# Kernel tuning notes

Hardware: AMD Instinct MI355X
Metric: run time of the kernel (lower is better)

Reference implementation:

```python
import jax, jax.numpy as jnp
import numpy as np

N, E, DIN, DH, DOUT = 50000, 800000, 128, 128, 64


def setup_inputs() -> dict:
    key = jax.random.key(0)
    ks = jax.random.split(key, 10)
    s = 0.05  # keep activations numerically sane
    return {
        "x": jax.random.normal(ks[0], (N, DIN), jnp.float32),
        "edge_index": jax.random.randint(ks[1], (2, E), 0, N, jnp.int64),
        "w_in": jax.random.normal(ks[2], (DIN, DH), jnp.float32) * s,
        "b_in": jnp.zeros((DH,), jnp.float32),
        "w_l0": jax.random.normal(ks[3], (DH, DH), jnp.float32) * s,
        "w_r0": jax.random.normal(ks[4], (DH, DH), jnp.float32) * s,
        "b0": jnp.zeros((DH,), jnp.float32),
        "w_l1": jax.random.normal(ks[5], (DH, DH), jnp.float32) * s,
        "w_r1": jax.random.normal(ks[6], (DH, DH), jnp.float32) * s,
        "b1": jnp.zeros((DH,), jnp.float32),
        "w_l2": jax.random.normal(ks[7], (DH, DOUT), jnp.float32) * s,
        "w_r2": jax.random.normal(ks[8], (DH, DOUT), jnp.float32) * s,
        "b2": jnp.zeros((DOUT,), jnp.float32),
    }


def _sage_conv(x, src, dst, w_l, w_r, b, n_nodes):
    # PyG SAGEConv (mean aggr): out = lin_l(mean_{j in N(i)} x_j) + lin_r(x_i)
    msg = x[src]  # [E, d] gather
    agg = jax.ops.segment_sum(msg, dst, num_segments=n_nodes)
    deg = jax.ops.segment_sum(jnp.ones((src.shape[0],), x.dtype), dst, num_segments=n_nodes)
    agg = agg / jnp.maximum(deg, 1.0)[:, None]  # isolated nodes -> 0
    return agg @ w_l + x @ w_r + b


def reference(x, edge_index, w_in, b_in, w_l0, w_r0, b0, w_l1, w_r1, b1, w_l2, w_r2, b2):
    src, dst = edge_index[0], edge_index[1]
    n = x.shape[0]
    h = x @ w_in + b_in
    inp = h
    h = jax.nn.relu(h)
    # conv 0 (hidden->hidden) + relu + (eval dropout = id) + residual
    h = _sage_conv(h, src, dst, w_l0, w_r0, b0, n)
    h = jax.nn.relu(h) + 0.2 * inp
    # conv 1 (hidden->hidden)
    h = _sage_conv(h, src, dst, w_l1, w_r1, b1, n)
    h = jax.nn.relu(h) + 0.2 * inp
    # conv 2 (hidden->out), no activation/residual
    h = _sage_conv(h, src, dst, w_l2, w_r2, b2, n)
    return jax.nn.log_softmax(h, axis=-1)
```

## Files before the change

kernel.cpp:

```cpp
#include <hip/hip_runtime.h>
#include <stdint.h>

#define NN 50000
#define NE 800000
#define NBIN 196
#define ABLK 196
#define EPB 4082
#define BCAP 6144

typedef __attribute__((ext_vector_type(8))) short short8;
typedef __attribute__((ext_vector_type(4))) float floatx4;

__device__ __forceinline__ uint16_t f2bf(float f){
  union { float f; uint32_t u; } c; c.f = f;
  uint32_t u = c.u + 0x7FFFu + ((c.u >> 16) & 1u);
  return (uint16_t)(u >> 16);
}
__device__ __forceinline__ float bflo(uint32_t v){
  union { uint32_t u; float f; } c; c.u = v << 16; return c.f;
}
__device__ __forceinline__ float bfhi(uint32_t v){
  union { uint32_t u; float f; } c; c.u = v & 0xFFFF0000u; return c.f;
}

#define B_CVT 6250
#define B_HIST ABLK
#define B_PIN 64
#define B_P0  128
#define B_P1  128
#define B_P2  64

__device__ __forceinline__ void pack_one(int idx, const float* __restrict__ wl,
                                         const float* __restrict__ wr,
                                         uint16_t* __restrict__ bp,
                                         int ncolL, int ncolR, int NT){
  int j = idx & 7, lane = (idx >> 3) & 63, rest = idx >> 9;
  int nt = rest % NT, kt = rest / NT;
  int k = kt * 32 + ((lane >> 4) << 3) + j;
  int n = nt * 16 + (lane & 15);
  float v = (n < ncolL) ? wl[k * ncolL + n] : wr[k * ncolR + (n - ncolL)];
  bp[idx] = f2bf(v);
}

__global__ __launch_bounds__(256) void k_prep(const float* __restrict__ x, uint2* __restrict__ xb,
                                              const int* __restrict__ ei, int* __restrict__ histG,
                                              const float* __restrict__ w_in,
                                              const float* __restrict__ w_l0, const float* __restrict__ w_r0,
                                              const float* __restrict__ w_l1, const float* __restrict__ w_r1,
                                              const float* __restrict__ w_l2, const float* __restrict__ w_r2,
                                              uint16_t* __restrict__ bpIn, uint16_t* __restrict__ bp0,
                                              uint16_t* __restrict__ bp1, uint16_t* __restrict__ bp2){
  __shared__ int hsh[NBIN];
  int b = blockIdx.x;
  if (b < B_CVT){
    int i = b * 256 + threadIdx.x;
    if (i < NN * 128 / 4){
      float4 v = ((const float4*)x)[i];
      uint32_t lo = (uint32_t)f2bf(v.x) | ((uint32_t)f2bf(v.y) << 16);
      uint32_t hi = (uint32_t)f2bf(v.z) | ((uint32_t)f2bf(v.w) << 16);
      xb[i] = make_uint2(lo, hi);
    }
    return;
  }
  b -= B_CVT;
  if (b < B_HIST){
    for (int i = threadIdx.x; i < NBIN; i += 256) hsh[i] = 0;
    __syncthreads();
    int base = b * EPB;
    for (int k = threadIdx.x; k < EPB; k += 256){
      int e = base + k;
      if (e < NE) atomicAdd(&hsh[ei[NE + e] >> 8], 1);
    }
    __syncthreads();
    for (int i = threadIdx.x; i < NBIN; i += 256) histG[b * NBIN + i] = hsh[i];
    return;
  }
  b -= B_HIST;
  if (b < B_PIN){ pack_one(b * 256 + threadIdx.x, w_in, w_in, bpIn, 128, 0, 8); return; }
  b -= B_PIN;
  if (b < B_P0){ pack_one(b * 256 + threadIdx.x, w_l0, w_r0, bp0, 128, 128, 16); return; }
  b -= B_P0;
  if (b < B_P1){ pack_one(b * 256 + threadIdx.x, w_l1, w_r1, bp1, 128, 128, 16); return; }
  b -= B_P1;
  pack_one(b * 256 + threadIdx.x, w_l2, w_r2, bp2, 64, 64, 8);
}

__global__ __launch_bounds__(256) void k_scanG(int* __restrict__ histG, int* __restrict__ binStart){
  __shared__ int s[256];
  int t = threadIdx.x;
  int tot = 0;
  if (t < NBIN){
    for (int b = 0; b < ABLK; ++b){
      int v = histG[b * NBIN + t];
      histG[b * NBIN + t] = tot;
      tot += v;
    }
  }
  s[t] = (t < NBIN) ? tot : 0;
  __syncthreads();
  #pragma unroll
  for (int off = 1; off < 256; off <<= 1){
    int u = (t >= off) ? s[t - off] : 0;
    __syncthreads();
    s[t] += u;
    __syncthreads();
  }
  int excl = s[t] - ((t < NBIN) ? tot : 0);
  if (t < NBIN){
    binStart[t] = excl;
    for (int b = 0; b < ABLK; ++b) histG[b * NBIN + t] += excl;
  }
  if (t == 0) binStart[NBIN] = NE;
}

__global__ __launch_bounds__(256) void k_bin(const int* __restrict__ ei, const int* __restrict__ histG,
                                             uint32_t* __restrict__ pairs){
  __shared__ int h[NBIN], loc[NBIN], cur[NBIN], gof[NBIN];
  __shared__ int sc[256];
  __shared__ uint32_t st[EPB];
  int t = threadIdx.x;
  int base = blockIdx.x * EPB;
  for (int i = t; i < NBIN; i += 256) h[i] = 0;
  __syncthreads();
  for (int k = t; k < EPB; k += 256){
    int e = base + k;
    if (e < NE) atomicAdd(&h[ei[NE + e] >> 8], 1);
  }
  __syncthreads();
  int cv = (t < NBIN) ? h[t] : 0;
  sc[t] = cv;
  __syncthreads();
  #pragma unroll
  for (int off = 1; off < 256; off <<= 1){
    int u = (t >= off) ? sc[t - off] : 0;
    __syncthreads();
    sc[t] += u;
    __syncthreads();
  }
  if (t < NBIN){
    int excl = sc[t] - cv;
    loc[t] = excl;
    cur[t] = excl;
    gof[t] = histG[blockIdx.x * NBIN + t];
  }
  __syncthreads();
  for (int k = t; k < EPB; k += 256){
    int e = base + k;
    if (e < NE){
      int d = ei[NE + e];
      int s0 = ei[e];
      int pos = atomicAdd(&cur[d >> 8], 1);
      st[pos] = (uint32_t)s0 | ((uint32_t)d << 16);
    }
  }
  __syncthreads();
  int cnt = min(EPB, NE - base);
  for (int k = t; k < cnt; k += 256){
    uint32_t v = st[k];
    int bin = (int)(v >> 24);
    pairs[gof[bin] + (k - loc[bin])] = v;
  }
}

__global__ __launch_bounds__(256) void k_csr(const uint32_t* __restrict__ pairs, const int* __restrict__ binStart,
                                             int* __restrict__ rowp, uint16_t* __restrict__ colx){
  __shared__ uint32_t pl[BCAP];
  __shared__ uint16_t stg[BCAP];
  __shared__ int h[256], sc[256];
  int i = blockIdx.x, t = threadIdx.x;
  int p0 = binStart[i], p1 = binStart[i + 1];
  int cnt = min(p1 - p0, BCAP);
  for (int k = t; k < cnt; k += 256) pl[k] = pairs[p0 + k];
  h[t] = 0;
  __syncthreads();
  for (int k = t; k < cnt; k += 256) atomicAdd(&h[(pl[k] >> 16) & 255], 1);
  __syncthreads();
  int cv = h[t];
  sc[t] = cv;
  __syncthreads();
  #pragma unroll
  for (int off = 1; off < 256; off <<= 1){
    int u = (t >= off) ? sc[t - off] : 0;
    __syncthreads();
    sc[t] += u;
    __syncthreads();
  }
  int excl = sc[t] - cv;
  int n0 = i << 8;
  int nc = min(256, NN - n0);
  if (t < nc) rowp[n0 + t] = p0 + excl;
  if (i == NBIN - 1 && t == 0) rowp[NN] = NE;
  h[t] = excl;
  __syncthreads();
  for (int k = t; k < cnt; k += 256){
    uint32_t v = pl[k];
    int pos = atomicAdd(&h[(v >> 16) & 255], 1);
    stg[pos] = (uint16_t)(v & 0xFFFFu);
  }
  __syncthreads();
  for (int k = t; k < cnt; k += 256) colx[p0 + k] = stg[k];
}

__global__ __launch_bounds__(256) void k_lin0(const uint16_t* __restrict__ xb,
                                              const uint16_t* __restrict__ BpIn, const float* __restrict__ b_in,
                                              const uint16_t* __restrict__ Bp0, const float* __restrict__ b0,
                                              uint16_t* __restrict__ resb, uint16_t* __restrict__ y0,
                                              uint16_t* __restrict__ z0){
  __shared__ uint16_t ash[16 * 136];
  int lane = threadIdx.x & 63, wave = threadIdx.x >> 6;
  short8 bIn[4][2], bC0[4][4];
  #pragma unroll
  for (int kt = 0; kt < 4; ++kt){
    #pragma unroll
    for (int n = 0; n < 2; ++n)
      bIn[kt][n] = *(const short8*)(BpIn + (size_t)((kt * 8 + wave * 2 + n) * 64 + lane) * 8);
    #pragma unroll
    for (int n = 0; n < 4; ++n)
      bC0[kt][n] = *(const short8*)(Bp0 + (size_t)((kt * 16 + wave * 4 + n) * 64 + lane) * 8);
  }
  int m = lane & 15, quad = lane >> 4;
  int r0 = blockIdx.x * 16;
  const uint16_t* arow = xb + (size_t)(r0 + m) * 128 + quad * 8;
  short8 af[4];
  #pragma unroll
  for (int kt = 0; kt < 4; ++kt) af[kt] = *(const short8*)(arow + kt * 32);
  floatx4 accH[2];
  #pragma unroll
  for (int n = 0; n < 2; ++n) accH[n] = (floatx4){0.f, 0.f, 0.f, 0.f};
  #pragma unroll
  for (int kt = 0; kt < 4; ++kt)
    #pragma unroll
    for (int n = 0; n < 2; ++n)
      accH[n] = __builtin_amdgcn_mfma_f32_16x16x32_bf16(af[kt], bIn[kt][n], accH[n], 0, 0, 0);
  int rbase = r0 + quad * 4;
  #pragma unroll
  for (int n = 0; n < 2; ++n){
    int c = (wave * 2 + n) * 16 + m;
    float bi = b_in[c];
    #pragma unroll
    for (int i = 0; i < 4; ++i){
      float hh = accH[n][i] + bi;
      int row = rbase + i;
      resb[(size_t)row * 128 + c] = f2bf(0.2f * hh);
      ash[(quad * 4 + i) * 136 + c] = f2bf(fmaxf(hh, 0.f));
    }
  }
  __syncthreads();
  short8 af2[4];
  #pragma unroll
  for (int kt = 0; kt < 4; ++kt)
    af2[kt] = *(const short8*)&ash[m * 136 + quad * 8 + kt * 32];
  floatx4 acc[4];
  #pragma unroll
  for (int n = 0; n < 4; ++n) acc[n] = (floatx4){0.f, 0.f, 0.f, 0.f};
  #pragma unroll
  for (int kt = 0; kt < 4; ++kt)
    #pragma unroll
    for (int n = 0; n < 4; ++n)
      acc[n] = __builtin_amdgcn_mfma_f32_16x16x32_bf16(af2[kt], bC0[kt][n], acc[n], 0, 0, 0);
  #pragma unroll
  for (int n = 0; n < 4; ++n){
    int c = (wave * 4 + n) * 16 + m;
    #pragma unroll
    for (int i = 0; i < 4; ++i){
      float v = acc[n][i];
      int row = rbase + i;
      if (c < 128) y0[(size_t)row * 128 + c] = f2bf(v);
      else         z0[(size_t)row * 128 + (c - 128)] = f2bf(v + b0[c - 128]);
    }
  }
}

template<int NTW, int MODE>
__global__ __launch_bounds__(256) void k_gemm(const uint16_t* __restrict__ A, const uint16_t* __restrict__ Bp,
                                              const float* __restrict__ bias,
                                              uint16_t* __restrict__ o0, uint16_t* __restrict__ o1,
                                              float* __restrict__ o2){
  const int NTT = 4 * NTW;
  int lane = threadIdx.x & 63;
  int wave = threadIdx.x >> 6;
  short8 bfrag[4][NTW];
  #pragma unroll
  for (int kt = 0; kt < 4; ++kt)
    #pragma unroll
    for (int n = 0; n < NTW; ++n)
      bfrag[kt][n] = *(const short8*)(Bp + (size_t)((kt * NTT + wave * NTW + n) * 64 + lane) * 8);

  int m = lane & 15, quad = lane >> 4;
  const int nrt = NN / 16;
  for (int rt = blockIdx.x; rt < nrt; rt += gridDim.x){
    int r0 = rt * 16;
    const uint16_t* arow = A + (size_t)(r0 + m) * 128 + quad * 8;
    short8 af[4];
    #pragma unroll
    for (int kt = 0; kt < 4; ++kt) af[kt] = *(const short8*)(arow + kt * 32);
    floatx4 acc[NTW];
    #pragma unroll
    for (int n = 0; n < NTW; ++n) acc[n] = (floatx4){0.f, 0.f, 0.f, 0.f};
    #pragma unroll
    for (int kt = 0; kt < 4; ++kt)
      #pragma unroll
      for (int n = 0; n < NTW; ++n)
        acc[n] = __builtin_amdgcn_mfma_f32_16x16x32_bf16(af[kt], bfrag[kt][n], acc[n], 0, 0, 0);

    int rbase = r0 + quad * 4;
    #pragma unroll
    for (int n = 0; n < NTW; ++n){
      int c = (wave * NTW + n) * 16 + m;
      #pragma unroll
      for (int i = 0; i < 4; ++i){
        float v = acc[n][i];
        int row = rbase + i;
        if (MODE == 1){
          if (c < 128) o0[(size_t)row * 128 + c] = f2bf(v);
          else         o1[(size_t)row * 128 + (c - 128)] = f2bf(v + bias[c - 128]);
        } else {
          if (c < 64) o0[(size_t)row * 64 + c] = f2bf(v);
          else        o2[(size_t)row * 64 + (c - 64)] = v + bias[c - 64];
        }
      }
    }
  }
}

__global__ __launch_bounds__(256) void agg_mid(const uint4* __restrict__ yb, const uint4* __restrict__ zb,
                                               const uint4* __restrict__ resb,
                                               const uint16_t* __restrict__ colx, const int* __restrict__ rowp,
                                               uint4* __restrict__ hb_out){
  int wid = blockIdx.x * 4 + (threadIdx.x >> 6);
  if (wid >= NN) return;
  int lane = threadIdx.x & 63;
  int q = lane >> 4, sub = lane & 15;
  int e0 = rowp[wid], e1 = rowp[wid + 1];
  float a0 = 0.f, a1 = 0.f, a2 = 0.f, a3 = 0.f, a4 = 0.f, a5 = 0.f, a6 = 0.f, a7 = 0.f;
  int e = e0 + q;
  for (; e + 12 < e1; e += 16){
    uint4 v0 = yb[(size_t)colx[e]      * 16 + sub];
    uint4 v1 = yb[(size_t)colx[e + 4]  * 16 + sub];
    uint4 v2 = yb[(size_t)colx[e + 8]  * 16 + sub];
    uint4 v3 = yb[(size_t)colx[e + 12] * 16 + sub];
    a0 += bflo(v0.x) + bflo(v1.x) + bflo(v2.x) + bflo(v3.x);
    a1 += bfhi(v0.x) + bfhi(v1.x) + bfhi(v2.x) + bfhi(v3.x);
    a2 += bflo(v0.y) + bflo(v1.y) + bflo(v2.y) + bflo(v3.y);
    a3 += bfhi(v0.y) + bfhi(v1.y) + bfhi(v2.y) + bfhi(v3.y);
    a4 += bflo(v0.z) + bflo(v1.z) + bflo(v2.z) + bflo(v3.z);
    a5 += bfhi(v0.z) + bfhi(v1.z) + bfhi(v2.z) + bfhi(v3.z);
    a6 += bflo(v0.w) + bflo(v1.w) + bflo(v2.w) + bflo(v3.w);
    a7 += bfhi(v0.w) + bfhi(v1.w) + bfhi(v2.w) + bfhi(v3.w);
  }
  for (; e < e1; e += 4){
    uint4 v = yb[(size_t)colx[e] * 16 + sub];
    a0 += bflo(v.x); a1 += bfhi(v.x); a2 += bflo(v.y); a3 += bfhi(v.y);
    a4 += bflo(v.z); a5 += bfhi(v.z); a6 += bflo(v.w); a7 += bfhi(v.w);
  }
  #pragma unroll
  for (int off = 16; off < 64; off <<= 1){
    a0 += __shfl_xor(a0, off, 64);
    a1 += __shfl_xor(a1, off, 64);
    a2 += __shfl_xor(a2, off, 64);
    a3 += __shfl_xor(a3, off, 64);
    a4 += __shfl_xor(a4, off, 64);
    a5 += __shfl_xor(a5, off, 64);
    a6 += __shfl_xor(a6, off, 64);
    a7 += __shfl_xor(a7, off, 64);
  }
  int deg = e1 - e0;
  float inv = deg > 0 ? 1.f / (float)deg : 0.f;
  if (q == 0){
    uint4 zv = zb[(size_t)wid * 16 + sub];
    uint4 rv = resb[(size_t)wid * 16 + sub];
    float w0 = fmaxf(a0 * inv + bflo(zv.x), 0.f) + bflo(rv.x);
    float w1 = fmaxf(a1 * inv + bfhi(zv.x), 0.f) + bfhi(rv.x);
    float w2 = fmaxf(a2 * inv + bflo(zv.y), 0.f) + bflo(rv.y);
    float w3 = fmaxf(a3 * inv + bfhi(zv.y), 0.f) + bfhi(rv.y);
    float w4 = fmaxf(a4 * inv + bflo(zv.z), 0.f) + bflo(rv.z);
    float w5 = fmaxf(a5 * inv + bfhi(zv.z), 0.f) + bfhi(rv.z);
    float w6 = fmaxf(a6 * inv + bflo(zv.w), 0.f) + bflo(rv.w);
    float w7 = fmaxf(a7 * inv + bfhi(zv.w), 0.f) + bfhi(rv.w);
    uint4 o;
    o.x = (uint32_t)f2bf(w0) | ((uint32_t)f2bf(w1) << 16);
    o.y = (uint32_t)f2bf(w2) | ((uint32_t)f2bf(w3) << 16);
    o.z = (uint32_t)f2bf(w4) | ((uint32_t)f2bf(w5) << 16);
    o.w = (uint32_t)f2bf(w6) | ((uint32_t)f2bf(w7) << 16);
    hb_out[(size_t)wid * 16 + sub] = o;
  }
}

__global__ __launch_bounds__(256) void agg_out(const uint2* __restrict__ yb2, const float* __restrict__ z2,
                                               const uint16_t* __restrict__ colx, const int* __restrict__ rowp,
                                               float* __restrict__ out){
  int wid = blockIdx.x * 4 + (threadIdx.x >> 6);
  if (wid >= NN) return;
  int lane = threadIdx.x & 63;
  int q = lane >> 4, sub = lane & 15;
  int e0 = rowp[wid], e1 = rowp[wid + 1];
  float a0 = 0.f, a1 = 0.f, a2 = 0.f, a3 = 0.f;
  int e = e0 + q;
  for (; e + 12 < e1; e += 16){
    uint2 v0 = yb2[(size_t)colx[e]      * 16 + sub];
    uint2 v1 = yb2[(size_t)colx[e + 4]  * 16 + sub];
    uint2 v2 = yb2[(size_t)colx[e + 8]  * 16 + sub];
    uint2 v3 = yb2[(size_t)colx[e + 12] * 16 + sub];
    a0 += bflo(v0.x) + bflo(v1.x) + bflo(v2.x) + bflo(v3.x);
    a1 += bfhi(v0.x) + bfhi(v1.x) + bfhi(v2.x) + bfhi(v3.x);
    a2 += bflo(v0.y) + bflo(v1.y) + bflo(v2.y) + bflo(v3.y);
    a3 += bfhi(v0.y) + bfhi(v1.y) + bfhi(v2.y) + bfhi(v3.y);
  }
  for (; e < e1; e += 4){
    uint2 v = yb2[(size_t)colx[e] * 16 + sub];
    a0 += bflo(v.x); a1 += bfhi(v.x); a2 += bflo(v.y); a3 += bfhi(v.y);
  }
  #pragma unroll
  for (int off = 16; off < 64; off <<= 1){
    a0 += __shfl_xor(a0, off, 64);
    a1 += __shfl_xor(a1, off, 64);
    a2 += __shfl_xor(a2, off, 64);
    a3 += __shfl_xor(a3, off, 64);
  }
  int deg = e1 - e0;
  float inv = deg > 0 ? 1.f / (float)deg : 0.f;
  float4 zv = ((const float4*)z2)[(size_t)wid * 16 + sub];
  float v0 = a0 * inv + zv.x;
  float v1 = a1 * inv + zv.y;
  float v2 = a2 * inv + zv.z;
  float v3 = a3 * inv + zv.w;
  float mx = fmaxf(fmaxf(v0, v1), fmaxf(v2, v3));
  #pragma unroll
  for (int off = 1; off < 16; off <<= 1) mx = fmaxf(mx, __shfl_xor(mx, off, 64));
  float sm = __expf(v0 - mx) + __expf(v1 - mx) + __expf(v2 - mx) + __expf(v3 - mx);
  #pragma unroll
  for (int off = 1; off < 16; off <<= 1) sm += __shfl_xor(sm, off, 64);
  if (q == 0){
    float ls = __logf(sm);
    float4 o = make_float4((v0 - mx) - ls, (v1 - mx) - ls, (v2 - mx) - ls, (v3 - mx) - ls);
    ((float4*)out)[(size_t)wid * 16 + sub] = o;
  }
}

extern "C" void kernel_launch(void* const* d_in, const int* in_sizes, int n_in,
                              void* d_out, int out_size, void* d_ws, size_t ws_size,
                              hipStream_t stream){
  const float* x    = (const float*)d_in[0];
  const int*   ei   = (const int*)d_in[1];
  const float* w_in = (const float*)d_in[2];
  const float* b_in = (const float*)d_in[3];
  const float* w_l0 = (const float*)d_in[4];
  const float* w_r0 = (const float*)d_in[5];
  const float* b0   = (const float*)d_in[6];
  const float* w_l1 = (const float*)d_in[7];
  const float* w_r1 = (const float*)d_in[8];
  const float* b1   = (const float*)d_in[9];
  const float* w_l2 = (const float*)d_in[10];
  const float* w_r2 = (const float*)d_in[11];
  const float* b2   = (const float*)d_in[12];
  float* out = (float*)d_out;

  char* ws = (char*)d_ws;
  size_t off = 0;
  auto take = [&](size_t bytes) -> char* {
    char* p = ws + off;
    off = (off + bytes + 1023) & ~(size_t)1023;
    return p;
  };
  uint16_t* xb   = (uint16_t*)take((size_t)NN * 128 * 2);
  uint16_t* hb   = (uint16_t*)take((size_t)NN * 128 * 2);
  uint16_t* resb = (uint16_t*)take((size_t)NN * 128 * 2);
  uint16_t* y0   = (uint16_t*)take((size_t)NN * 128 * 2);
  uint16_t* z0   = (uint16_t*)take((size_t)NN * 128 * 2);
  uint32_t* pairs = (uint32_t*)take((size_t)NE * 4);
  uint16_t* colx  = (uint16_t*)take((size_t)NE * 2);
  int* histG    = (int*)take((size_t)NBIN * ABLK * 4);
  int* binStart = (int*)take((size_t)(NBIN + 1) * 4);
  int* rowp     = (int*)take((size_t)(NN + 1) * 4);
  uint16_t* BpIn = (uint16_t*)take(128 * 128 * 2);
  uint16_t* Bp0  = (uint16_t*)take(128 * 256 * 2);
  uint16_t* Bp1  = (uint16_t*)take(128 * 256 * 2);
  uint16_t* Bp2  = (uint16_t*)take(128 * 128 * 2);
  uint16_t* y2 = y0;
  float*    z2 = (float*)z0;
  (void)ws_size; (void)in_sizes; (void)n_in; (void)out_size;

  k_prep<<<B_CVT + B_HIST + B_PIN + B_P0 + B_P1 + B_P2, 256, 0, stream>>>(
      x, (uint2*)xb, ei, histG, w_in, w_l0, w_r0, w_l1, w_r1, w_l2, w_r2, BpIn, Bp0, Bp1, Bp2);

  k_scanG<<<1, 256, 0, stream>>>(histG, binStart);
  k_bin<<<ABLK, 256, 0, stream>>>(ei, histG, pairs);
  k_csr<<<NBIN, 256, 0, stream>>>(pairs, binStart, rowp, colx);

  k_lin0<<<NN / 16, 256, 0, stream>>>(xb, BpIn, b_in, Bp0, b0, resb, y0, z0);

  agg_mid<<<NN / 4, 256, 0, stream>>>((const uint4*)y0, (const uint4*)z0, (const uint4*)resb,
                                      colx, rowp, (uint4*)hb);
  k_gemm<4, 1><<<1024, 256, 0, stream>>>(hb, Bp1, b1, y0, z0, nullptr);

  agg_mid<<<NN / 4, 256, 0, stream>>>((const uint4*)y0, (const uint4*)z0, (const uint4*)resb,
                                      colx, rowp, (uint4*)hb);
  k_gemm<2, 2><<<1024, 256, 0, stream>>>(hb, Bp2, b2, y2, nullptr, z2);

  agg_out<<<NN / 4, 256, 0, stream>>>((const uint2*)y2, z2, colx, rowp, out);
}
```

Measured before the change: 300.9 us.

## Fuse edge binning with first linear layer and drop bf16 input conversion pass

```diff
diff --git a/kernel.cpp b/kernel.cpp
--- a/kernel.cpp
+++ b/kernel.cpp
@@ -23,7 +23,6 @@
   union { uint32_t u; float f; } c; c.u = v & 0xFFFF0000u; return c.f;
 }
 
-#define B_CVT 6250
 #define B_HIST ABLK
 #define B_PIN 64
 #define B_P0  128
@@ -42,8 +41,7 @@
   bp[idx] = f2bf(v);
 }
 
-__global__ __launch_bounds__(256) void k_prep(const float* __restrict__ x, uint2* __restrict__ xb,
-                                              const int* __restrict__ ei, int* __restrict__ histG,
+__global__ __launch_bounds__(256) void k_prep(const int* __restrict__ ei, int* __restrict__ histG,
                                               const float* __restrict__ w_in,
                                               const float* __restrict__ w_l0, const float* __restrict__ w_r0,
                                               const float* __restrict__ w_l1, const float* __restrict__ w_r1,
@@ -52,17 +50,6 @@
                                               uint16_t* __restrict__ bp1, uint16_t* __restrict__ bp2){
   __shared__ int hsh[NBIN];
   int b = blockIdx.x;
-  if (b < B_CVT){
-    int i = b * 256 + threadIdx.x;
-    if (i < NN * 128 / 4){
-      float4 v = ((const float4*)x)[i];
-      uint32_t lo = (uint32_t)f2bf(v.x) | ((uint32_t)f2bf(v.y) << 16);
-      uint32_t hi = (uint32_t)f2bf(v.z) | ((uint32_t)f2bf(v.w) << 16);
-      xb[i] = make_uint2(lo, hi);
-    }
-    return;
-  }
-  b -= B_CVT;
   if (b < B_HIST){
     for (int i = threadIdx.x; i < NBIN; i += 256) hsh[i] = 0;
     __syncthreads();
@@ -85,16 +72,14 @@
   pack_one(b * 256 + threadIdx.x, w_l2, w_r2, bp2, 64, 64, 8);
 }
 
-__global__ __launch_bounds__(256) void k_scanG(int* __restrict__ histG, int* __restrict__ binStart){
+__global__ __launch_bounds__(256) void k_scanG(const int* __restrict__ histG, int* __restrict__ binStart,
+                                               int* __restrict__ binCur){
   __shared__ int s[256];
   int t = threadIdx.x;
   int tot = 0;
   if (t < NBIN){
-    for (int b = 0; b < ABLK; ++b){
-      int v = histG[b * NBIN + t];
-      histG[b * NBIN + t] = tot;
-      tot += v;
-    }
+    #pragma unroll 4
+    for (int b = 0; b < ABLK; ++b) tot += histG[b * NBIN + t];
   }
   s[t] = (t < NBIN) ? tot : 0;
   __syncthreads();
@@ -108,57 +93,144 @@
   int excl = s[t] - ((t < NBIN) ? tot : 0);
   if (t < NBIN){
     binStart[t] = excl;
-    for (int b = 0; b < ABLK; ++b) histG[b * NBIN + t] += excl;
+    binCur[t * 16] = excl;
   }
   if (t == 0) binStart[NBIN] = NE;
 }
 
-__global__ __launch_bounds__(256) void k_bin(const int* __restrict__ ei, const int* __restrict__ histG,
-                                             uint32_t* __restrict__ pairs){
-  __shared__ int h[NBIN], loc[NBIN], cur[NBIN], gof[NBIN];
-  __shared__ int sc[256];
-  __shared__ uint32_t st[EPB];
+#define B_BIN 196
+#define SMSZ 20488
+
+__global__ __launch_bounds__(256) void k_mid(const int* __restrict__ ei, int* __restrict__ binCur,
+                                             uint32_t* __restrict__ pairs,
+                                             const float* __restrict__ x,
+                                             const uint16_t* __restrict__ BpIn, const float* __restrict__ b_in,
+                                             const uint16_t* __restrict__ Bp0, const float* __restrict__ b0,
+                                             uint16_t* __restrict__ resb, uint16_t* __restrict__ y0,
+                                             uint16_t* __restrict__ z0){
+  __shared__ __align__(16) char smraw[SMSZ];
   int t = threadIdx.x;
-  int base = blockIdx.x * EPB;
-  for (int i = t; i < NBIN; i += 256) h[i] = 0;
-  __syncthreads();
-  for (int k = t; k < EPB; k += 256){
-    int e = base + k;
-    if (e < NE) atomicAdd(&h[ei[NE + e] >> 8], 1);
-  }
-  __syncthreads();
-  int cv = (t < NBIN) ? h[t] : 0;
-  sc[t] = cv;
-  __syncthreads();
-  #pragma unroll
-  for (int off = 1; off < 256; off <<= 1){
-    int u = (t >= off) ? sc[t - off] : 0;
-    __syncthreads();
-    sc[t] += u;
-    __syncthreads();
-  }
-  if (t < NBIN){
-    int excl = sc[t] - cv;
-    loc[t] = excl;
-    cur[t] = excl;
-    gof[t] = histG[blockIdx.x * NBIN + t];
-  }
-  __syncthreads();
-  for (int k = t; k < EPB; k += 256){
-    int e = base + k;
-    if (e < NE){
-      int d = ei[NE + e];
-      int s0 = ei[e];
-      int pos = atomicAdd(&cur[d >> 8], 1);
-      st[pos] = (uint32_t)s0 | ((uint32_t)d << 16);
-    }
-  }
-  __syncthreads();
-  int cnt = min(EPB, NE - base);
-  for (int k = t; k < cnt; k += 256){
-    uint32_t v = st[k];
-    int bin = (int)(v >> 24);
-    pairs[gof[bin] + (k - loc[bin])] = v;
+  if (blockIdx.x < B_BIN){
+    int* h   = (int*)smraw;
+    int* loc = h + NBIN;
+    int* cur = loc + NBIN;
+    int* gof = cur + NBIN;
+    int* sc  = gof + NBIN;
+    uint32_t* st = (uint32_t*)(sc + 256);
+    int base = blockIdx.x * EPB;
+    for (int i = t; i < NBIN; i += 256) h[i] = 0;
+    __syncthreads();
+    for (int k = t; k < EPB; k += 256){
+      int e = base + k;
+      if (e < NE) atomicAdd(&h[ei[NE + e] >> 8], 1);
+    }
+    __syncthreads();
+    int cv = (t < NBIN) ? h[t] : 0;
+    sc[t] = cv;
+    __syncthreads();
+    #pragma unroll
+    for (int off = 1; off < 256; off <<= 1){
+      int u = (t >= off) ? sc[t - off] : 0;
+      __syncthreads();
+      sc[t] += u;
+      __syncthreads();
+    }
+    if (t < NBIN){
+      int excl = sc[t] - cv;
+      loc[t] = excl;
+      cur[t] = excl;
+      if (cv) gof[t] = atomicAdd(&binCur[t * 16], cv);
+    }
+    __syncthreads();
+    for (int k = t; k < EPB; k += 256){
+      int e = base + k;
+      if (e < NE){
+        int d = ei[NE + e];
+        int s0 = ei[e];
+        int pos = atomicAdd(&cur[d >> 8], 1);
+        st[pos] = (uint32_t)s0 | ((uint32_t)d << 16);
+      }
+    }
+    __syncthreads();
+    int cnt = min(EPB, NE - base);
+    for (int k = t; k < cnt; k += 256){
+      uint32_t v = st[k];
+      int bin = (int)(v >> 24);
+      pairs[gof[bin] + (k - loc[bin])] = v;
+    }
+    return;
+  }
+  uint16_t* ash = (uint16_t*)smraw;
+  int lane = t & 63, wave = t >> 6;
+  short8 bIn[4][2], bC0[4][4];
+  #pragma unroll
+  for (int kt = 0; kt < 4; ++kt){
+    #pragma unroll
+    for (int n = 0; n < 2; ++n)
+      bIn[kt][n] = *(const short8*)(BpIn + (size_t)((kt * 8 + wave * 2 + n) * 64 + lane) * 8);
+    #pragma unroll
+    for (int n = 0; n < 4; ++n)
+      bC0[kt][n] = *(const short8*)(Bp0 + (size_t)((kt * 16 + wave * 4 + n) * 64 + lane) * 8);
+  }
+  int m = lane & 15, quad = lane >> 4;
+  int r0 = (blockIdx.x - B_BIN) * 16;
+  const float* xrow = x + (size_t)(r0 + m) * 128 + quad * 8;
+  short8 af[4];
+  #pragma unroll
+  for (int kt = 0; kt < 4; ++kt){
+    float4 p = *(const float4*)(xrow + kt * 32);
+    float4 q2 = *(const float4*)(xrow + kt * 32 + 4);
+    short8 a;
+    a[0] = (short)f2bf(p.x);  a[1] = (short)f2bf(p.y);
+    a[2] = (short)f2bf(p.z);  a[3] = (short)f2bf(p.w);
+    a[4] = (short)f2bf(q2.x); a[5] = (short)f2bf(q2.y);
+    a[6] = (short)f2bf(q2.z); a[7] = (short)f2bf(q2.w);
+    af[kt] = a;
+  }
+  floatx4 accH[2];
+  #pragma unroll
+  for (int n = 0; n < 2; ++n) accH[n] = (floatx4){0.f, 0.f, 0.f, 0.f};
+  #pragma unroll
+  for (int kt = 0; kt < 4; ++kt)
+    #pragma unroll
+    for (int n = 0; n < 2; ++n)
+      accH[n] = __builtin_amdgcn_mfma_f32_16x16x32_bf16(af[kt], bIn[kt][n], accH[n], 0, 0, 0);
+  int rbase = r0 + quad * 4;
+  #pragma unroll
+  for (int n = 0; n < 2; ++n){
+    int c = (wave * 2 + n) * 16 + m;
+    float bi = b_in[c];
+    #pragma unroll
+    for (int i = 0; i < 4; ++i){
+      float hh = accH[n][i] + bi;
+      int row = rbase + i;
+      resb[(size_t)row * 128 + c] = f2bf(0.2f * hh);
+      ash[(quad * 4 + i) * 136 + c] = f2bf(fmaxf(hh, 0.f));
+    }
+  }
+  __syncthreads();
+  short8 af2[4];
+  #pragma unroll
+  for (int kt = 0; kt < 4; ++kt)
+    af2[kt] = *(const short8*)&ash[m * 136 + quad * 8 + kt * 32];
+  floatx4 acc[4];
+  #pragma unroll
+  for (int n = 0; n < 4; ++n) acc[n] = (floatx4){0.f, 0.f, 0.f, 0.f};
+  #pragma unroll
+  for (int kt = 0; kt < 4; ++kt)
+    #pragma unroll
+    for (int n = 0; n < 4; ++n)
+      acc[n] = __builtin_amdgcn_mfma_f32_16x16x32_bf16(af2[kt], bC0[kt][n], acc[n], 0, 0, 0);
+  #pragma unroll
+  for (int n = 0; n < 4; ++n){
+    int c = (wave * 4 + n) * 16 + m;
+    #pragma unroll
+    for (int i = 0; i < 4; ++i){
+      float v = acc[n][i];
+      int row = rbase + i;
+      if (c < 128) y0[(size_t)row * 128 + c] = f2bf(v);
+      else         z0[(size_t)row * 128 + (c - 128)] = f2bf(v + b0[c - 128]);
+    }
   }
 }
 
@@ -199,76 +271,6 @@
   }
   __syncthreads();
   for (int k = t; k < cnt; k += 256) colx[p0 + k] = stg[k];
-}
-
-__global__ __launch_bounds__(256) void k_lin0(const uint16_t* __restrict__ xb,
-                                              const uint16_t* __restrict__ BpIn, const float* __restrict__ b_in,
-                                              const uint16_t* __restrict__ Bp0, const float* __restrict__ b0,
-                                              uint16_t* __restrict__ resb, uint16_t* __restrict__ y0,
-                                              uint16_t* __restrict__ z0){
-  __shared__ uint16_t ash[16 * 136];
-  int lane = threadIdx.x & 63, wave = threadIdx.x >> 6;
-  short8 bIn[4][2], bC0[4][4];
-  #pragma unroll
-  for (int kt = 0; kt < 4; ++kt){
-    #pragma unroll
-    for (int n = 0; n < 2; ++n)
-      bIn[kt][n] = *(const short8*)(BpIn + (size_t)((kt * 8 + wave * 2 + n) * 64 + lane) * 8);
-    #pragma unroll
-    for (int n = 0; n < 4; ++n)
-      bC0[kt][n] = *(const short8*)(Bp0 + (size_t)((kt * 16 + wave * 4 + n) * 64 + lane) * 8);
-  }
-  int m = lane & 15, quad = lane >> 4;
-  int r0 = blockIdx.x * 16;
-  const uint16_t* arow = xb + (size_t)(r0 + m) * 128 + quad * 8;
-  short8 af[4];
-  #pragma unroll
-  for (int kt = 0; kt < 4; ++kt) af[kt] = *(const short8*)(arow + kt * 32);
-  floatx4 accH[2];
-  #pragma unroll
-  for (int n = 0; n < 2; ++n) accH[n] = (floatx4){0.f, 0.f, 0.f, 0.f};
-  #pragma unroll
-  for (int kt = 0; kt < 4; ++kt)
-    #pragma unroll
-    for (int n = 0; n < 2; ++n)
-      accH[n] = __builtin_amdgcn_mfma_f32_16x16x32_bf16(af[kt], bIn[kt][n], accH[n], 0, 0, 0);
-  int rbase = r0 + quad * 4;
-  #pragma unroll
-  for (int n = 0; n < 2; ++n){
-    int c = (wave * 2 + n) * 16 + m;
-    float bi = b_in[c];
-    #pragma unroll
-    for (int i = 0; i < 4; ++i){
-      float hh = accH[n][i] + bi;
-      int row = rbase + i;
-      resb[(size_t)row * 128 + c] = f2bf(0.2f * hh);
-      ash[(quad * 4 + i) * 136 + c] = f2bf(fmaxf(hh, 0.f));
-    }
-  }
-  __syncthreads();
-  short8 af2[4];
-  #pragma unroll
-  for (int kt = 0; kt < 4; ++kt)
-    af2[kt] = *(const short8*)&ash[m * 136 + quad * 8 + kt * 32];
-  floatx4 acc[4];
-  #pragma unroll
-  for (int n = 0; n < 4; ++n) acc[n] = (floatx4){0.f, 0.f, 0.f, 0.f};
-  #pragma unroll
-  for (int kt = 0; kt < 4; ++kt)
-    #pragma unroll
-    for (int n = 0; n < 4; ++n)
-      acc[n] = __builtin_amdgcn_mfma_f32_16x16x32_bf16(af2[kt], bC0[kt][n], acc[n], 0, 0, 0);
-  #pragma unroll
-  for (int n = 0; n < 4; ++n){
-    int c = (wave * 4 + n) * 16 + m;
-    #pragma unroll
-    for (int i = 0; i < 4; ++i){
-      float v = acc[n][i];
-      int row = rbase + i;
-      if (c < 128) y0[(size_t)row * 128 + c] = f2bf(v);
-      else         z0[(size_t)row * 128 + (c - 128)] = f2bf(v + b0[c - 128]);
-    }
-  }
 }
 
 template<int NTW, int MODE>
@@ -462,7 +464,6 @@
     off = (off + bytes + 1023) & ~(size_t)1023;
     return p;
   };
-  uint16_t* xb   = (uint16_t*)take((size_t)NN * 128 * 2);
   uint16_t* hb   = (uint16_t*)take((size_t)NN * 128 * 2);
   uint16_t* resb = (uint16_t*)take((size_t)NN * 128 * 2);
   uint16_t* y0   = (uint16_t*)take((size_t)NN * 128 * 2);
@@ -471,6 +472,7 @@
   uint16_t* colx  = (uint16_t*)take((size_t)NE * 2);
   int* histG    = (int*)take((size_t)NBIN * ABLK * 4);
   int* binStart = (int*)take((size_t)(NBIN + 1) * 4);
+  int* binCur   = (int*)take((size_t)NBIN * 16 * 4);
   int* rowp     = (int*)take((size_t)(NN + 1) * 4);
   uint16_t* BpIn = (uint16_t*)take(128 * 128 * 2);
   uint16_t* Bp0  = (uint16_t*)take(128 * 256 * 2);
@@ -480,14 +482,14 @@
   float*    z2 = (float*)z0;
   (void)ws_size; (void)in_sizes; (void)n_in; (void)out_size;
 
-  k_prep<<<B_CVT + B_HIST + B_PIN + B_P0 + B_P1 + B_P2, 256, 0, stream>>>(
-      x, (uint2*)xb, ei, histG, w_in, w_l0, w_r0, w_l1, w_r1, w_l2, w_r2, BpIn, Bp0, Bp1, Bp2);
-
-  k_scanG<<<1, 256, 0, stream>>>(histG, binStart);
-  k_bin<<<ABLK, 256, 0, stream>>>(ei, histG, pairs);
+  k_prep<<<B_HIST + B_PIN + B_P0 + B_P1 + B_P2, 256, 0, stream>>>(
+      ei, histG, w_in, w_l0, w_r0, w_l1, w_r1, w_l2, w_r2, BpIn, Bp0, Bp1, Bp2);
+
+  k_scanG<<<1, 256, 0, stream>>>(histG, binStart, binCur);
+
+  k_mid<<<B_BIN + NN / 16, 256, 0, stream>>>(ei, binCur, pairs, x, BpIn, b_in, Bp0, b0, resb, y0, z0);
+
   k_csr<<<NBIN, 256, 0, stream>>>(pairs, binStart, rowp, colx);
-
-  k_lin0<<<NN / 16, 256, 0, stream>>>(xb, BpIn, b_in, Bp0, b0, resb, y0, z0);
 
   agg_mid<<<NN / 4, 256, 0, stream>>>((const uint4*)y0, (const uint4*)z0, (const uint4*)resb,
                                       colx, rowp, (uint4*)hb);
```

Measured after the change: 289.4 us. 1.04x faster.
